# Kernel tuning notes

Measured on AMD Instinct MI355X. Metric: run time of the kernel, lower is better.

The kernel has to match this reference:

```python
import jax, jax.numpy as jnp
import numpy as np


def setup_inputs() -> dict:
    key = jax.random.key(0)
    kx, kw, kb = jax.random.split(key, 3)
    x = jax.random.normal(kx, (32, 256, 64, 64), dtype=jnp.float32)
    # Conv2d(in=2, out=1, kernel=7) weights, OIHW layout
    W = jax.random.normal(kw, (1, 2, 7, 7), dtype=jnp.float32) * 0.1
    b = jax.random.normal(kb, (1,), dtype=jnp.float32) * 0.1
    return {"x": x, "W": W, "b": b}


def reference(x, W, b):
    # Channel-wise max and mean pooling -> [B, 1, H, W] each
    maxpool = jnp.max(x, axis=1, keepdims=True)
    avgpool = jnp.mean(x, axis=1, keepdims=True)
    pool = jnp.concatenate([maxpool, avgpool], axis=1)  # [B, 2, H, W]
    # 7x7 conv, stride 1, padding 3 (SAME), NCHW / OIHW
    samap = jax.lax.conv_general_dilated(
        pool, W,
        window_strides=(1, 1),
        padding=[(3, 3), (3, 3)],
        dimension_numbers=("NCHW", "OIHW", "NCHW"),
    ) + b[None, :, None, None]
    samap = jax.nn.sigmoid(samap)  # [B, 1, H, W]
    return x * samap
```

## Files before the change

### kernel.cpp

```cpp
#include <hip/hip_runtime.h>
#include <math.h>

constexpr int B_  = 32;
constexpr int C_  = 256;
constexpr int H_  = 64;
constexpr int W_  = 64;
constexpr int HW_ = H_ * W_;
constexpr size_t CHW_ = (size_t)C_ * HW_;

typedef float v4f __attribute__((ext_vector_type(4)));

__global__ __launch_bounds__(512) void sam_fused(const float* __restrict__ x,
                                                 const float* __restrict__ Wp,
                                                 const float* __restrict__ bp,
                                                 float* __restrict__ out) {
    const int hwid = blockIdx.x;
    const int blk  = (hwid & 7) * 64 + (hwid >> 3);
    const int b    = blk >> 4;
    const int h0   = (blk & 15) * 4;
    const int tid  = threadIdx.x;
    const int wv   = tid >> 6;
    const int lane = tid & 63;

    __shared__ float sw[98];
    __shared__ __align__(16) float spool[2][10][64];
    __shared__ __align__(16) float ssa[256];

    if (tid < 98) sw[tid] = Wp[tid];

    const int g = lane & 15;
    const int s = lane >> 4;
    for (int r = wv; r < 10; r += 8) {
        const int hh = h0 + r - 3;
        if (hh >= 0 && hh < H_) {
            const float* base = x + (size_t)b * CHW_ + (size_t)(s * 64) * HW_
                                  + hh * W_ + g * 4;
            float4 v  = *(const float4*)base;
            float4 mx = v, sm = v;
#pragma unroll 16
            for (int c = 1; c < 64; ++c) {
                float4 u = *(const float4*)(base + (size_t)c * HW_);
                mx.x = fmaxf(mx.x, u.x); mx.y = fmaxf(mx.y, u.y);
                mx.z = fmaxf(mx.z, u.z); mx.w = fmaxf(mx.w, u.w);
                sm.x += u.x; sm.y += u.y; sm.z += u.z; sm.w += u.w;
            }
#pragma unroll
            for (int m = 16; m <= 32; m <<= 1) {
                mx.x = fmaxf(mx.x, __shfl_xor(mx.x, m));
                mx.y = fmaxf(mx.y, __shfl_xor(mx.y, m));
                mx.z = fmaxf(mx.z, __shfl_xor(mx.z, m));
                mx.w = fmaxf(mx.w, __shfl_xor(mx.w, m));
                sm.x += __shfl_xor(sm.x, m);
                sm.y += __shfl_xor(sm.y, m);
                sm.z += __shfl_xor(sm.z, m);
                sm.w += __shfl_xor(sm.w, m);
            }
            if (s == 0) {
                const float inv = 1.0f / 256.0f;
                *(float4*)&spool[0][r][g * 4] = mx;
                *(float4*)&spool[1][r][g * 4] =
                    make_float4(sm.x * inv, sm.y * inv, sm.z * inv, sm.w * inv);
            }
        } else if (s == 0) {
            const float4 z = make_float4(0.f, 0.f, 0.f, 0.f);
            *(float4*)&spool[0][r][g * 4] = z;
            *(float4*)&spool[1][r][g * 4] = z;
        }
    }
    __syncthreads();

    if (tid < 256) {
        const int r   = tid >> 6;
        const int col = tid & 63;
        float acc = bp[0];
#pragma unroll
        for (int p = 0; p < 2; ++p) {
            const float* wc = sw + p * 49;
#pragma unroll
            for (int kh = 0; kh < 7; ++kh) {
                const float* prow = &spool[p][r + kh][0];
#pragma unroll
                for (int kw = 0; kw < 7; ++kw) {
                    const int ww = col + kw - 3;
                    if (ww >= 0 && ww < W_)
                        acc = fmaf(prow[ww], wc[kh * 7 + kw], acc);
                }
            }
        }
        ssa[tid] = 1.0f / (1.0f + expf(-acc));
    }
    __syncthreads();

    const float4 sv = ((const float4*)ssa)[lane];
    const size_t rowbase = (size_t)b * CHW_ + (size_t)h0 * W_ + lane * 4;
    for (int c = wv; c < C_; c += 8) {
        const float* xb = x + rowbase + (size_t)c * HW_;
        float*       ob = out + rowbase + (size_t)c * HW_;
        const float4 xv = *(const float4*)xb;
        v4f ov;
        ov.x = xv.x * sv.x; ov.y = xv.y * sv.y;
        ov.z = xv.z * sv.z; ov.w = xv.w * sv.w;
        __builtin_nontemporal_store(ov, (v4f*)ob);
    }
}

extern "C" void kernel_launch(void* const* d_in, const int* in_sizes, int n_in,
                              void* d_out, int out_size, void* d_ws, size_t ws_size,
                              hipStream_t stream) {
    const float* x  = (const float*)d_in[0];
    const float* Wp = (const float*)d_in[1];
    const float* bp = (const float*)d_in[2];
    float* out = (float*)d_out;
    (void)d_ws; (void)ws_size;

    sam_fused<<<B_ * (H_ / 4), 512, 0, stream>>>(x, Wp, bp, out);
}
```

Baseline: 254.7 us.

## Keep block's own rows in registers to avoid rereading x for output

Each thread now loads its 32 float4 slices of the block's four output rows into registers once. These registers feed both the channel max/mean for the center rows (combined across waves through shared memory) and the final scaling, so the second global read of x is gone. Six waves still compute the halo rows directly from global memory. The cost is 128 extra VGPRs per thread, which cuts occupancy and may cause spills at 512 threads per block.

```diff
diff --git a/kernel.cpp b/kernel.cpp
--- a/kernel.cpp
+++ b/kernel.cpp
@@ -23,23 +23,32 @@
     const int lane = tid & 63;
 
     __shared__ float sw[98];
-    __shared__ __align__(16) float spool[2][10][64];
-    __shared__ __align__(16) float ssa[256];
+    __shared__ __align__(16) float4 lmax[8][64];
+    __shared__ __align__(16) float4 lsum[8][64];
+    __shared__ __align__(16) float  spool[2][10][64];
+    __shared__ __align__(16) float  ssa[256];
 
     if (tid < 98) sw[tid] = Wp[tid];
 
-    const int g = lane & 15;
-    const int s = lane >> 4;
-    for (int r = wv; r < 10; r += 8) {
+    const size_t spanbase = (size_t)b * CHW_ + (size_t)h0 * W_ + lane * 4;
+    float4 xr[32];
+#pragma unroll
+    for (int k = 0; k < 32; ++k)
+        xr[k] = *(const float4*)(x + spanbase + (size_t)(wv + 8 * k) * HW_);
+
+    if (wv < 6) {
+        const int r  = (wv < 3) ? wv : wv + 4;
         const int hh = h0 + r - 3;
+        const int g  = lane & 15;
+        const int s  = lane >> 4;
         if (hh >= 0 && hh < H_) {
-            const float* base = x + (size_t)b * CHW_ + (size_t)(s * 64) * HW_
-                                  + hh * W_ + g * 4;
-            float4 v  = *(const float4*)base;
+            const float* basep = x + (size_t)b * CHW_ + (size_t)(s * 64) * HW_
+                                   + hh * W_ + g * 4;
+            float4 v  = *(const float4*)basep;
             float4 mx = v, sm = v;
 #pragma unroll 16
             for (int c = 1; c < 64; ++c) {
-                float4 u = *(const float4*)(base + (size_t)c * HW_);
+                float4 u = *(const float4*)(basep + (size_t)c * HW_);
                 mx.x = fmaxf(mx.x, u.x); mx.y = fmaxf(mx.y, u.y);
                 mx.z = fmaxf(mx.z, u.z); mx.w = fmaxf(mx.w, u.w);
                 sm.x += u.x; sm.y += u.y; sm.z += u.z; sm.w += u.w;
@@ -67,6 +76,36 @@
             *(float4*)&spool[1][r][g * 4] = z;
         }
     }
+
+    {
+        float4 mx = xr[0], sm = xr[0];
+#pragma unroll
+        for (int k = 1; k < 32; ++k) {
+            mx.x = fmaxf(mx.x, xr[k].x); mx.y = fmaxf(mx.y, xr[k].y);
+            mx.z = fmaxf(mx.z, xr[k].z); mx.w = fmaxf(mx.w, xr[k].w);
+            sm.x += xr[k].x; sm.y += xr[k].y; sm.z += xr[k].z; sm.w += xr[k].w;
+        }
+        lmax[wv][lane] = mx;
+        lsum[wv][lane] = sm;
+    }
+    __syncthreads();
+
+    if (tid < 64) {
+        float4 M = lmax[0][tid], S = lsum[0][tid];
+#pragma unroll
+        for (int g2 = 1; g2 < 8; ++g2) {
+            float4 m2 = lmax[g2][tid], s2 = lsum[g2][tid];
+            M.x = fmaxf(M.x, m2.x); M.y = fmaxf(M.y, m2.y);
+            M.z = fmaxf(M.z, m2.z); M.w = fmaxf(M.w, m2.w);
+            S.x += s2.x; S.y += s2.y; S.z += s2.z; S.w += s2.w;
+        }
+        const float inv = 1.0f / 256.0f;
+        const int r   = tid >> 4;
+        const int col = (tid & 15) * 4;
+        *(float4*)&spool[0][3 + r][col] = M;
+        *(float4*)&spool[1][3 + r][col] =
+            make_float4(S.x * inv, S.y * inv, S.z * inv, S.w * inv);
+    }
     __syncthreads();
 
     if (tid < 256) {
@@ -92,15 +131,13 @@
     __syncthreads();
 
     const float4 sv = ((const float4*)ssa)[lane];
-    const size_t rowbase = (size_t)b * CHW_ + (size_t)h0 * W_ + lane * 4;
-    for (int c = wv; c < C_; c += 8) {
-        const float* xb = x + rowbase + (size_t)c * HW_;
-        float*       ob = out + rowbase + (size_t)c * HW_;
-        const float4 xv = *(const float4*)xb;
+#pragma unroll
+    for (int k = 0; k < 32; ++k) {
         v4f ov;
-        ov.x = xv.x * sv.x; ov.y = xv.y * sv.y;
-        ov.z = xv.z * sv.z; ov.w = xv.w * sv.w;
-        __builtin_nontemporal_store(ov, (v4f*)ob);
+        ov.x = xr[k].x * sv.x; ov.y = xr[k].y * sv.y;
+        ov.z = xr[k].z * sv.z; ov.w = xr[k].w * sv.w;
+        __builtin_nontemporal_store(ov,
+            (v4f*)(out + spanbase + (size_t)(wv + 8 * k) * HW_));
     }
 }
 
```

After: 251.0 us. No clear change (-1.5%).
